# Kernel tuning notes

Measured on AMD Instinct MI355X. Metric: run time of the kernel, lower is better.

## Reference

```python
import jax, jax.numpy as jnp
import numpy as np

N, E, D, C = 100000, 200000, 32, 8
H = 2 * C * C          # 128, MLP hidden
OUT = 4 * C * C + 4 * C  # 288, MLP output


def setup_inputs() -> dict:
    key = jax.random.key(0)
    ks = jax.random.split(key, 10)
    return {
        "x": jax.random.normal(ks[0], (N, D, C), jnp.float32),
        "edge_index": jax.random.randint(ks[1], (2, E), 0, N, jnp.int64),
        "edge_features_a": jax.random.normal(ks[2], (E, D, C), jnp.float32),
        "edge_features_b": jax.random.normal(ks[3], (E, D, C), jnp.float32),
        "edge_matrices": jax.random.normal(ks[4], (E, D, D), jnp.float32),
        "W1": jax.random.normal(ks[5], (H, H), jnp.float32) / np.sqrt(H),
        "b1": jnp.zeros((H,), jnp.float32),
        "ln_g": jnp.ones((H,), jnp.float32),
        "ln_b": jnp.zeros((H,), jnp.float32),
        "W2": jax.random.normal(ks[6], (H, OUT), jnp.float32) / np.sqrt(H),
        "b2": jnp.zeros((OUT,), jnp.float32),
    }


def _matrix_norm(w):
    # unit Frobenius norm over last two dims (MatrixNormalization, scale=1)
    n = jnp.sqrt(jnp.sum(w * w, axis=(-2, -1), keepdims=True))
    return w / (n + 1e-6)


def reference(x, edge_index, edge_features_a, edge_features_b, edge_matrices,
              W1, b1, ln_g, ln_b, W2, b2):
    c = x.shape[-1]
    x_node_a = x[edge_index[0]]                     # [E, D, C]
    x_node_b = x[edge_index[1]]                     # [E, D, C]

    edge_overlap = jnp.einsum('eij,eic,ejm->ecm', edge_matrices,
                              edge_features_a, edge_features_b)  # [E, C, C]
    node_overlap = jnp.einsum('eij,eic,ejm->ecm', edge_matrices,
                              x_node_a, x_node_b)                # [E, C, C]

    h = jnp.concatenate([edge_overlap.reshape(edge_overlap.shape[0], -1),
                         node_overlap.reshape(node_overlap.shape[0], -1)], axis=-1)
    h = jax.nn.silu(h @ W1 + b1)
    mu = jnp.mean(h, axis=-1, keepdims=True)
    var = jnp.var(h, axis=-1, keepdims=True)
    h = (h - mu) / jnp.sqrt(var + 1e-5) * ln_g + ln_b
    mlp_res = h @ W2 + b2                           # [E, 4C^2 + 4C]

    weights = mlp_res[:, :4 * c * c]
    factors = mlp_res[:, 4 * c * c:]
    ew_a, ew_b, nw_a, nw_b = jnp.split(weights, 4, axis=-1)
    ew_a = _matrix_norm(ew_a.reshape(-1, c, c))
    ew_b = _matrix_norm(ew_b.reshape(-1, c, c))
    nw_a = _matrix_norm(nw_a.reshape(-1, c, c))
    nw_b = _matrix_norm(nw_b.reshape(-1, c, c))

    f_ea = factors[:, None, 0 * c:1 * c]
    f_eb = factors[:, None, 1 * c:2 * c]
    f_na = factors[:, None, 2 * c:3 * c]
    f_nb = factors[:, None, 3 * c:4 * c]

    x_edge_a = (f_ea * (edge_features_a @ ew_a) + f_na * (x_node_a @ nw_a)) / 2
    x_edge_b = (f_eb * (edge_features_b @ ew_b) + f_nb * (x_node_b @ nw_b)) / 2
    return (x_edge_a, x_edge_b)
```

## Files before the change

### kernel.cpp

```cpp
#include <hip/hip_runtime.h>
#include <hip/hip_fp16.h>

typedef _Float16 f16;
typedef _Float16 half8 __attribute__((ext_vector_type(8)));
typedef _Float16 half4 __attribute__((ext_vector_type(4)));
typedef float f32x4 __attribute__((ext_vector_type(4)));
typedef int   int4v __attribute__((ext_vector_type(4)));

static __device__ __forceinline__ void fence_lds(){
  asm volatile("s_waitcnt lgkmcnt(0)" ::: "memory");
  __builtin_amdgcn_sched_barrier(0);
}

__global__ void k0_convert(const float* __restrict__ W1, const float* __restrict__ W2,
                           f16* __restrict__ W1T, f16* __restrict__ W2T){
  int o = blockIdx.x*256 + threadIdx.x;
  if (o < 128*128){
    int j = o >> 7, i = o & 127;
    W1T[o] = (f16)W1[i*128 + j];
  } else {
    int o2 = o - 128*128;
    int n = o2 >> 7, i = o2 & 127;
    W2T[o2] = (f16)W2[i*288 + n];
  }
}

struct ERegs { f32x4 a, b, xa, xb, m0, m1, m2, m3; };

static __device__ __forceinline__ ERegs load_edge_i(
    const float* __restrict__ x,
    const float* __restrict__ efa, const float* __restrict__ efb,
    const float* __restrict__ em, int e, int ia, int ib, int l){
  ERegs r;
  const size_t eb = (size_t)e * 256;
  r.a  = *(const f32x4*)(efa + eb + l*4);
  r.b  = *(const f32x4*)(efb + eb + l*4);
  r.xa = *(const f32x4*)(x + (size_t)ia*256 + l*4);
  r.xb = *(const f32x4*)(x + (size_t)ib*256 + l*4);
  const size_t mb = (size_t)e * 1024;
  r.m0 = *(const f32x4*)(em + mb +   0 + l*4);
  r.m1 = *(const f32x4*)(em + mb + 256 + l*4);
  r.m2 = *(const f32x4*)(em + mb + 512 + l*4);
  r.m3 = *(const f32x4*)(em + mb + 768 + l*4);
  return r;
}

__global__ __launch_bounds__(256, 3) void k_fused(
    const float* __restrict__ x, const int* __restrict__ eidx,
    const float* __restrict__ efa, const float* __restrict__ efb,
    const float* __restrict__ em,
    const f16* __restrict__ W1T, const f16* __restrict__ W2T,
    const float* __restrict__ b1, const float* __restrict__ lng,
    const float* __restrict__ lnb, const float* __restrict__ b2,
    float* __restrict__ outA, float* outB, int E)
{
  __shared__ f16   sWk[17024];
  __shared__ f16   sH0[16*128];
  __shared__ f16   sH1[16*128];
  __shared__ float sStat[128];

  const int tid = threadIdx.x;
  const int l = tid & 63, w = tid >> 6, q = l >> 4, n16 = l & 15;
  const int e0 = blockIdx.x * 16;

  f16* Mb   = sWk + w*3200;
  f16* AXT  = Mb + 1280;
  f16* BXT  = AXT + 640;
  f16* MBXT = BXT + 640;

  half4 hA[4], hXa[4], hB[4], hXb[4];

  const int ew = e0 + w*4;
  int4v iav = *(const int4v*)(eidx + ew);
  int4v ibv = *(const int4v*)(eidx + E + ew);

  ERegs buf0 = load_edge_i(x, efa, efb, em, ew,     iav[0], ibv[0], l);
  ERegs buf1 = load_edge_i(x, efa, efb, em, ew + 1, iav[1], ibv[1], l);
  ERegs buf2 = load_edge_i(x, efa, efb, em, ew + 2, iav[2], ibv[2], l);
  #pragma unroll
  for (int i = 0; i < 4; ++i){
    const int le = w*4 + i;
    ERegs nxt3;
    if (i < 1) nxt3 = load_edge_i(x, efa, efb, em, ew + 3, iav[3], ibv[3], l);

    {
      int d = l >> 1, cb = (l & 1)*4;
      half4 ta, txa, tb, txb;
      #pragma unroll
      for (int j = 0; j < 4; ++j){
        int c = cb + j;
        f16 va  = (f16)buf0.a[j],  vxa = (f16)buf0.xa[j];
        f16 vb  = (f16)buf0.b[j],  vxb = (f16)buf0.xb[j];
        AXT[c*40 + d]     = va;   AXT[(8+c)*40 + d] = vxa;
        BXT[c*40 + d]     = vb;   BXT[(8+c)*40 + d] = vxb;
        ta[j] = va; txa[j] = vxa; tb[j] = vb; txb[j] = vxb;
      }
      hA[i] = ta; hXa[i] = txa; hB[i] = tb; hXb[i] = txb;
      int r0 = l >> 3, c0 = (l & 7)*4;
      f16* p0 = Mb + ( 0 + r0)*40 + c0;
      p0[0]=(f16)buf0.m0[0]; p0[1]=(f16)buf0.m0[1]; p0[2]=(f16)buf0.m0[2]; p0[3]=(f16)buf0.m0[3];
      f16* p1 = Mb + ( 8 + r0)*40 + c0;
      p1[0]=(f16)buf0.m1[0]; p1[1]=(f16)buf0.m1[1]; p1[2]=(f16)buf0.m1[2]; p1[3]=(f16)buf0.m1[3];
      f16* p2 = Mb + (16 + r0)*40 + c0;
      p2[0]=(f16)buf0.m2[0]; p2[1]=(f16)buf0.m2[1]; p2[2]=(f16)buf0.m2[2]; p2[3]=(f16)buf0.m2[3];
      f16* p3 = Mb + (24 + r0)*40 + c0;
      p3[0]=(f16)buf0.m3[0]; p3[1]=(f16)buf0.m3[1]; p3[2]=(f16)buf0.m3[2]; p3[3]=(f16)buf0.m3[3];
    }
    fence_lds();

    half8 bF  = *(half8*)(BXT + n16*40 + q*8);
    half8 aF0 = *(half8*)(Mb  + n16*40      + q*8);
    half8 aF1 = *(half8*)(Mb  + (16+n16)*40 + q*8);
    f32x4 z = {0.f,0.f,0.f,0.f};
    f32x4 d0 = __builtin_amdgcn_mfma_f32_16x16x32_f16(aF0, bF, z, 0,0,0);
    f32x4 d1 = __builtin_amdgcn_mfma_f32_16x16x32_f16(aF1, bF, z, 0,0,0);
    {
      f16* p0 = MBXT + n16*40 + q*4;
      p0[0]=(f16)d0[0]; p0[1]=(f16)d0[1]; p0[2]=(f16)d0[2]; p0[3]=(f16)d0[3];
      f16* p1 = MBXT + n16*40 + 16 + q*4;
      p1[0]=(f16)d1[0]; p1[1]=(f16)d1[1]; p1[2]=(f16)d1[2]; p1[3]=(f16)d1[3];
    }
    fence_lds();

    half8 aF2 = *(half8*)(AXT  + n16*40 + q*8);
    half8 bF2 = *(half8*)(MBXT + n16*40 + q*8);
    f32x4 d2 = __builtin_amdgcn_mfma_f32_16x16x32_f16(aF2, bF2, z, 0,0,0);

    if (q < 2 && n16 < 8){
      #pragma unroll
      for (int j=0;j<4;++j){
        int ch = 4*q + j;
        sH0[le*128 + ((ch ^ (le & 7))*8) + n16] = (f16)d2[j];
      }
    }
    if (q >= 2 && n16 >= 8){
      #pragma unroll
      for (int j=0;j<4;++j){
        int ch = 8 + 4*(q-2) + j;
        sH0[le*128 + ((ch ^ (le & 7))*8) + (n16-8)] = (f16)d2[j];
      }
    }
    buf0 = buf1; buf1 = buf2;
    if (i < 1) buf2 = nxt3;
    fence_lds();
  }
  __syncthreads();

  f32x4 acc[2] = {{0,0,0,0},{0,0,0,0}};
  #pragma unroll
  for (int ks = 0; ks < 4; ++ks){
    half8 aF = *(const half8*)(sH0 + n16*128 + (((ks*4 + q) ^ (n16 & 7))*8));
    #pragma unroll
    for (int c2 = 0; c2 < 2; ++c2){
      int ct = 2*w + c2;
      half8 bF = *(const half8*)(W1T + (size_t)(ct*16 + n16)*128 + ks*32 + q*8);
      acc[c2] = __builtin_amdgcn_mfma_f32_16x16x32_f16(aF, bF, acc[c2], 0,0,0);
    }
  }
  float sv[2][4];
  #pragma unroll
  for (int c2=0;c2<2;++c2)
    #pragma unroll
    for (int j=0;j<4;++j){
      int col = (2*w + c2)*16 + n16;
      float v = acc[c2][j] + b1[col];
      sv[c2][j] = v / (1.f + __expf(-v));
    }
  #pragma unroll
  for (int j=0;j<4;++j){
    float s  = sv[0][j] + sv[1][j];
    float sq = sv[0][j]*sv[0][j] + sv[1][j]*sv[1][j];
    #pragma unroll
    for (int m=1;m<16;m<<=1){ s += __shfl_xor(s, m, 64); sq += __shfl_xor(sq, m, 64); }
    if (n16 == 0){ sStat[(w*16 + 4*q + j)*2] = s; sStat[(w*16 + 4*q + j)*2 + 1] = sq; }
  }
  __syncthreads();
  float mu[4], rs[4];
  #pragma unroll
  for (int j=0;j<4;++j){
    int row = 4*q + j;
    float s=0.f, sq=0.f;
    #pragma unroll
    for (int w2=0;w2<4;++w2){ s += sStat[(w2*16+row)*2]; sq += sStat[(w2*16+row)*2+1]; }
    float m_ = s * (1.f/128.f);
    mu[j] = m_;
    rs[j] = rsqrtf(sq * (1.f/128.f) - m_*m_ + 1e-5f);
  }
  #pragma unroll
  for (int c2=0;c2<2;++c2)
    #pragma unroll
    for (int j=0;j<4;++j){
      int col = (2*w + c2)*16 + n16;
      int row = 4*q + j;
      float hn = (sv[c2][j] - mu[j])*rs[j]*lng[col] + lnb[col];
      sH1[row*128 + (((col>>3) ^ (row&7))*8) + (col&7)] = (f16)hn;
    }
  __syncthreads();

  float* sR = (float*)sWk;
  f32x4 acc2[5] = {{0,0,0,0},{0,0,0,0},{0,0,0,0},{0,0,0,0},{0,0,0,0}};
  #pragma unroll
  for (int ks=0;ks<4;++ks){
    half8 aF = *(const half8*)(sH1 + n16*128 + (((ks*4 + q) ^ (n16 & 7))*8));
    #pragma unroll
    for (int t=0;t<5;++t){
      int ct = w + 4*t;
      if (ct < 18){
        half8 bF = *(const half8*)(W2T + (size_t)(ct*16 + n16)*128 + ks*32 + q*8);
        acc2[t] = __builtin_amdgcn_mfma_f32_16x16x32_f16(aF, bF, acc2[t], 0,0,0);
      }
    }
  }
  #pragma unroll
  for (int t=0;t<5;++t){
    int ct = w + 4*t;
    if (ct < 18){
      #pragma unroll
      for (int j=0;j<4;++j){
        int col = ct*16 + n16, row = 4*q + j;
        sR[row*292 + col] = acc2[t][j] + b2[col];
      }
    }
  }
  __syncthreads();

  f16* pw    = sWk + 9344 + w*1920;
  f16* LHSst = pw;
  f16* RT    = pw + 1280;
  #pragma unroll
  for (int i = 0; i < 4; ++i){
    const int le = w*4 + i;
    const int e  = e0 + le;
    f32x4 w4 = *(const f32x4*)(sR + le*292 + l*4);
    float ssq = w4[0]*w4[0] + w4[1]*w4[1] + w4[2]*w4[2] + w4[3]*w4[3];
    #pragma unroll
    for (int m=1;m<16;m<<=1) ssq += __shfl_xor(ssq, m, 64);
    float rn = 1.f / (sqrtf(ssq) + 1e-6f);
    {
      uint32_t* z32 = (uint32_t*)RT;
      z32[l] = 0u; z32[l+64] = 0u; z32[l+128] = 0u; z32[l+192] = 0u; z32[l+256] = 0u;
    }
    const int mm = l >> 4;
    const int kk = n16 >> 1;
    #pragma unroll
    for (int j=0;j<4;++j){
      int c = (l & 1)*4 + j;
      float f = sR[le*292 + 256 + mm*8 + c];
      f16 val = (f16)(w4[j] * rn * f * 0.5f);
      int nOut = c + (mm & 1)*8;
      int rk   = kk + ((mm & 1) << 4) + ((mm >> 1) << 3);
      RT[nOut*40 + rk] = val;
    }
    {
      int d = l >> 1, cb = (l & 1)*4;
      *(half4*)(LHSst + d*40 + cb)      = hA[i];
      *(half4*)(LHSst + d*40 + 8 + cb)  = hXa[i];
      *(half4*)(LHSst + d*40 + 16 + cb) = hB[i];
      *(half4*)(LHSst + d*40 + 24 + cb) = hXb[i];
    }
    fence_lds();
    half8 bF = *(const half8*)(RT + n16*40 + q*8);
    f32x4 z = {0.f,0.f,0.f,0.f};
    const size_t eb = (size_t)e * 256;
    float* obase = (n16 < 8) ? (outA + eb + n16) : (outB + eb + n16 - 8);
    #pragma unroll
    for (int rt=0;rt<2;++rt){
      half8 aF = *(const half8*)(LHSst + (rt*16 + n16)*40 + q*8);
      f32x4 Dv = __builtin_amdgcn_mfma_f32_16x16x32_f16(aF, bF, z, 0,0,0);
      #pragma unroll
      for (int j=0;j<4;++j){
        int dR = rt*16 + 4*q + j;
        obase[dR*8] = Dv[j];
      }
    }
    fence_lds();
  }
}

extern "C" void kernel_launch(void* const* d_in, const int* in_sizes, int n_in,
                              void* d_out, int out_size, void* d_ws, size_t ws_size,
                              hipStream_t stream) {
  const float* x   = (const float*)d_in[0];
  const int*   ei  = (const int*)  d_in[1];
  const float* efa = (const float*)d_in[2];
  const float* efb = (const float*)d_in[3];
  const float* em  = (const float*)d_in[4];
  const float* W1  = (const float*)d_in[5];
  const float* b1  = (const float*)d_in[6];
  const float* lng = (const float*)d_in[7];
  const float* lnb = (const float*)d_in[8];
  const float* W2  = (const float*)d_in[9];
  const float* b2  = (const float*)d_in[10];
  const int E = in_sizes[1] / 2;

  float* outA = (float*)d_out;
  float* outB = outA + (size_t)E*256;
  f16* W1T = (f16*)d_ws;
  f16* W2T = W1T + 128*128;

  k0_convert<<<208, 256, 0, stream>>>(W1, W2, W1T, W2T);
  k_fused<<<E/16, 256, 0, stream>>>(x, ei, efa, efb, em, W1T, W2T,
                                    b1, lng, lnb, b2, outA, outB, E);
}
```

Before: 418.8 us.

## Pass intermediate MFMA result via cross-lane shuffles and prefetch W1 fragments

Drops the LDS round-trip (store plus fence plus reload) for the M·Bx intermediate. The fp16-packed accumulator values are now redistributed across lanes with __shfl so they form the B operand of the next MFMA directly. It also hoists the W1T fragment loads out of the post-loop GEMM and issues them early, so their global latency overlaps the edge-processing loop. This costs extra registers (8 half8 fragments) and shuffle instructions, which may reduce occupancy.

```diff
diff --git a/kernel.cpp b/kernel.cpp
--- a/kernel.cpp
+++ b/kernel.cpp
@@ -4,12 +4,19 @@
 typedef _Float16 f16;
 typedef _Float16 half8 __attribute__((ext_vector_type(8)));
 typedef _Float16 half4 __attribute__((ext_vector_type(4)));
+typedef _Float16 half2v __attribute__((ext_vector_type(2)));
 typedef float f32x4 __attribute__((ext_vector_type(4)));
 typedef int   int4v __attribute__((ext_vector_type(4)));
 
 static __device__ __forceinline__ void fence_lds(){
   asm volatile("s_waitcnt lgkmcnt(0)" ::: "memory");
   __builtin_amdgcn_sched_barrier(0);
+}
+
+static __device__ __forceinline__ int pack2(float a, float b){
+  union { half2v h; int i; } u;
+  u.h = (half2v){(f16)a, (f16)b};
+  return u.i;
 }
 
 __global__ void k0_convert(const float* __restrict__ W1, const float* __restrict__ W2,
@@ -66,7 +73,6 @@
   f16* Mb   = sWk + w*3200;
   f16* AXT  = Mb + 1280;
   f16* BXT  = AXT + 640;
-  f16* MBXT = BXT + 640;
 
   half4 hA[4], hXa[4], hB[4], hXb[4];
 
@@ -77,6 +83,17 @@
   ERegs buf0 = load_edge_i(x, efa, efb, em, ew,     iav[0], ibv[0], l);
   ERegs buf1 = load_edge_i(x, efa, efb, em, ew + 1, iav[1], ibv[1], l);
   ERegs buf2 = load_edge_i(x, efa, efb, em, ew + 2, iav[2], ibv[2], l);
+
+  half8 w1f[2][4];
+  #pragma unroll
+  for (int c2 = 0; c2 < 2; ++c2)
+    #pragma unroll
+    for (int ks = 0; ks < 4; ++ks)
+      w1f[c2][ks] = *(const half8*)(W1T + (size_t)(((2*w + c2)*16 + n16))*128 + ks*32 + q*8);
+
+  const int srcA = ((l & 16) ? 32 : 0) + n16;
+  const int srcB = srcA + 16;
+
   #pragma unroll
   for (int i = 0; i < 4; ++i){
     const int le = w*4 + i;
@@ -114,16 +131,22 @@
     f32x4 z = {0.f,0.f,0.f,0.f};
     f32x4 d0 = __builtin_amdgcn_mfma_f32_16x16x32_f16(aF0, bF, z, 0,0,0);
     f32x4 d1 = __builtin_amdgcn_mfma_f32_16x16x32_f16(aF1, bF, z, 0,0,0);
-    {
-      f16* p0 = MBXT + n16*40 + q*4;
-      p0[0]=(f16)d0[0]; p0[1]=(f16)d0[1]; p0[2]=(f16)d0[2]; p0[3]=(f16)d0[3];
-      f16* p1 = MBXT + n16*40 + 16 + q*4;
-      p1[0]=(f16)d1[0]; p1[1]=(f16)d1[1]; p1[2]=(f16)d1[2]; p1[3]=(f16)d1[3];
-    }
-    fence_lds();
-
-    half8 aF2 = *(half8*)(AXT  + n16*40 + q*8);
-    half8 bF2 = *(half8*)(MBXT + n16*40 + q*8);
+
+    int i00 = pack2(d0[0], d0[1]), i01 = pack2(d0[2], d0[3]);
+    int i10 = pack2(d1[0], d1[1]), i11 = pack2(d1[2], d1[3]);
+    int a00 = __shfl(i00, srcA, 64), a01 = __shfl(i01, srcA, 64);
+    int b00 = __shfl(i00, srcB, 64), b01 = __shfl(i01, srcB, 64);
+    int a10 = __shfl(i10, srcA, 64), a11 = __shfl(i11, srcA, 64);
+    int b10 = __shfl(i10, srcB, 64), b11 = __shfl(i11, srcB, 64);
+    const bool lo = (q < 2);
+    union { int i[4]; half8 h; } bu;
+    bu.i[0] = lo ? a00 : a10;
+    bu.i[1] = lo ? a01 : a11;
+    bu.i[2] = lo ? b00 : b10;
+    bu.i[3] = lo ? b01 : b11;
+    half8 bF2 = bu.h;
+
+    half8 aF2 = *(half8*)(AXT + n16*40 + q*8);
     f32x4 d2 = __builtin_amdgcn_mfma_f32_16x16x32_f16(aF2, bF2, z, 0,0,0);
 
     if (q < 2 && n16 < 8){
@@ -152,9 +175,7 @@
     half8 aF = *(const half8*)(sH0 + n16*128 + (((ks*4 + q) ^ (n16 & 7))*8));
     #pragma unroll
     for (int c2 = 0; c2 < 2; ++c2){
-      int ct = 2*w + c2;
-      half8 bF = *(const half8*)(W1T + (size_t)(ct*16 + n16)*128 + ks*32 + q*8);
-      acc[c2] = __builtin_amdgcn_mfma_f32_16x16x32_f16(aF, bF, acc[c2], 0,0,0);
+      acc[c2] = __builtin_amdgcn_mfma_f32_16x16x32_f16(aF, w1f[c2][ks], acc[c2], 0,0,0);
     }
   }
   float sv[2][4];
```

New measurement: 478.1 us. 1.14x slower.
